# Kernel optimization log

Hardware: AMD Instinct MI355X
Metric: run time of the kernel (lower is better)

The kernel has to match this reference:

```python
import jax, jax.numpy as jnp
import numpy as np

OUT = 7               # adaptive max pool output size (7,7)
SPATIAL_SCALE = 1.0 / 16.0


def _adaptive_bins(offset, length, grid_len):
    """Boolean masks [OUT, grid_len] for AdaptiveMaxPool2d bin membership.

    Torch adaptive pooling: bin i covers [floor(i*L/OUT), ceil((i+1)*L/OUT)).
    offset/length are traced int32 scalars (ROI start and extent on the grid).
    """
    i = jnp.arange(OUT, dtype=jnp.int32)
    starts = offset + (i * length) // OUT                      # inclusive
    ends = offset + ((i + 1) * length + (OUT - 1)) // OUT      # exclusive (ceil)
    g = jnp.arange(grid_len, dtype=jnp.int32)
    return (g[None, :] >= starts[:, None]) & (g[None, :] < ends[:, None])


def _pool_one_roi(fmap, roi):
    """fmap: [C, H, W] float; roi: [4] int32 (x1, y1, x2, y2) in feature coords.

    Equivalent to features[:, :, y1:y2+1, x1:x2+1] followed by
    AdaptiveMaxPool2d((7,7)). Returns [C, OUT, OUT].
    """
    C, H, W = fmap.shape
    x1, y1, x2, y2 = roi[0], roi[1], roi[2], roi[3]
    h_len = y2 - y1 + 1   # torch slice y1:y2+1
    w_len = x2 - x1 + 1
    mask_h = _adaptive_bins(y1, h_len, H)   # [OUT, H]
    mask_w = _adaptive_bins(x1, w_len, W)   # [OUT, W]
    neg = jnp.finfo(fmap.dtype).min
    # reduce W first: [C, H, OUT]
    col = jnp.where(mask_w[None, None, :, :], fmap[:, :, None, :], neg).max(-1)
    # then reduce H: [C, OUT(h), OUT(w)]
    out = jnp.where(mask_h[None, :, :, None], col[:, None, :, :], neg).max(2)
    return out


def roi_pool(features, rois):
    # features: [1, C, H, W]; rois: [R, 4] int32 image-pixel (x1, y1, x2, y2)
    fmap = features[0]
    # rois.float().mul_(spatial_scale).long(): truncation == floor for coords >= 0
    rois_f = (rois.astype(features.dtype) * SPATIAL_SCALE).astype(jnp.int32)
    # sequential map over ROIs keeps the masked-max intermediate per-ROI sized
    return jax.lax.map(lambda r: _pool_one_roi(fmap, r), rois_f)  # [R, C, 7, 7]


def setup_inputs() -> dict:
    key = jax.random.key(0)
    k1, k2, k3, k4, k5 = jax.random.split(key, 5)
    C, H, W, R = 512, 64, 64, 1024
    features = jax.random.normal(k1, (1, C, H, W), dtype=jnp.float32)
    img = H * 16  # 1024 px image
    x1 = jax.random.randint(k2, (R,), 0, img - 128, dtype=jnp.int32)
    y1 = jax.random.randint(k3, (R,), 0, img - 128, dtype=jnp.int32)
    bw = jax.random.randint(k4, (R,), 16, 128, dtype=jnp.int32)
    bh = jax.random.randint(k5, (R,), 16, 128, dtype=jnp.int32)
    rois = jnp.stack([x1, y1, x1 + bw, y1 + bh], axis=1)  # [R, 4], in-bounds
    return {"features": features, "rois": rois}


def reference(features, rois):
    return roi_pool(features, rois)
```

## Files before the change

kernel.cpp:

```cpp
#include <hip/hip_runtime.h>
#include <float.h>

constexpr int CC = 512, HH = 64, WW = 64, HW = HH * WW;
#define NEG (-FLT_MAX)
typedef float f4 __attribute__((ext_vector_type(4)));

__global__ __launch_bounds__(256) void transpose_kernel(
    const float* __restrict__ f, float* __restrict__ ft)
{
    __shared__ float tile[64][65];
    int bc = blockIdx.x & 7;
    int bs = blockIdx.x >> 3;
    int tx = threadIdx.x & 63, ty0 = threadIdx.x >> 6;
#pragma unroll
    for (int k = 0; k < 16; ++k) {
        int c = k * 4 + ty0;
        tile[c][tx] = __builtin_nontemporal_load(
            &f[(size_t)(bc * 64 + c) * HW + bs * 64 + tx]);
    }
    __syncthreads();
#pragma unroll
    for (int k = 0; k < 16; ++k) {
        int s = k * 4 + ty0;
        ft[(size_t)(bs * 64 + s) * CC + bc * 64 + tx] = tile[tx][s];
    }
}

#define KMIN(j) ((2 * (j)) / 7)
#define KMAX(j) ((9 * ((j) + 1) + 6) / 7)

__global__ __launch_bounds__(256) void pool_kernel(
    const float* __restrict__ ft,
    const int4*  __restrict__ rois,
    float* __restrict__ out,
    int nblocks)
{
    __shared__ __align__(16) float lds[4][32 * 49];
    int wslot = threadIdx.x >> 6;
    int b = __builtin_amdgcn_readfirstlane(blockIdx.x);
    if (b >= nblocks) return;
    int lane = threadIdx.x & 63;

    int bc = b & 7;
    int g  = b >> 3;
    int r  = g * 4 + wslot;
    int c0 = bc << 6;

    int4 roi = rois[r];
    int x1 = roi.x >> 4, y1 = roi.y >> 4, x2 = roi.z >> 4, y2 = roi.w >> 4;
    int hl = y2 - y1 + 1, wl = x2 - x1 + 1;

    int hs[7], he[7], s_[7], e_[7];
#pragma unroll
    for (int i = 0; i < 7; ++i) {
        hs[i] = y1 + (i * hl) / 7;
        he[i] = y1 + ((i + 1) * hl + 6) / 7;
        s_[i] = (i * wl) / 7;
        e_[i] = ((i + 1) * wl + 6) / 7;
    }

    float acc[7][7];
#pragma unroll
    for (int i = 0; i < 7; ++i)
#pragma unroll
        for (int j = 0; j < 7; ++j) acc[i][j] = NEG;

    const float* fb = ft + c0 + lane;
    for (int h = y1; h <= y2; ++h) {
        const float* rowp = fb + (size_t)h * (WW * CC);
        float v[9];
#pragma unroll
        for (int k = 0; k < 9; ++k) {
            v[k] = NEG;
            if (k < wl)
                v[k] = rowp[(x1 + k) * CC];
        }
        float m[7];
#pragma unroll
        for (int j = 0; j < 7; ++j) {
            float a = NEG;
#pragma unroll
            for (int k = KMIN(j); k < KMAX(j); ++k) {
                bool p = (k >= s_[j]) && (k < e_[j]);
                a = fmaxf(a, p ? v[k] : NEG);
            }
            m[j] = a;
        }
#pragma unroll
        for (int i = 0; i < 7; ++i) {
            if (h >= hs[i] && h < he[i]) {
#pragma unroll
                for (int j = 0; j < 7; ++j)
                    acc[i][j] = fmaxf(acc[i][j], m[j]);
            }
        }
    }

    float* L  = lds[wslot];
    float* ob = out + ((size_t)r * CC + c0) * 49;
#pragma unroll
    for (int round = 0; round < 2; ++round) {
        if ((lane >> 5) == round) {
            float* p = L + (lane & 31) * 49;
#pragma unroll
            for (int i = 0; i < 7; ++i)
#pragma unroll
                for (int j = 0; j < 7; ++j) p[i * 7 + j] = acc[i][j];
        }
        asm volatile("s_waitcnt lgkmcnt(0)" ::: "memory");
        float* og = ob + round * 1568;
#pragma unroll
        for (int s = 0; s < 6; ++s) {
            int idx = s * 64 + lane;
            __builtin_nontemporal_store(*(const f4*)(L + idx * 4),
                                        (f4*)(og + idx * 4));
        }
        if (lane < 8) {
            int idx = 384 + lane;
            __builtin_nontemporal_store(*(const f4*)(L + idx * 4),
                                        (f4*)(og + idx * 4));
        }
        asm volatile("s_waitcnt lgkmcnt(0)" ::: "memory");
    }
}

__global__ __launch_bounds__(256) void roi_pool_direct(
    const float* __restrict__ features, const int4* __restrict__ rois,
    float* __restrict__ out, int ngroups)
{
    int wid = __builtin_amdgcn_readfirstlane(
        blockIdx.x * (blockDim.x >> 6) + (threadIdx.x >> 6));
    if (wid >= ngroups) return;
    int lane = threadIdx.x & 63;
    if (lane >= 49) return;
    int r = wid >> 4, c0 = (wid & 15) * 32;
    int4 roi = rois[r];
    int x1 = roi.x >> 4, y1 = roi.y >> 4, x2 = roi.z >> 4, y2 = roi.w >> 4;
    int h_len = y2 - y1 + 1, w_len = x2 - x1 + 1;
    int oh = lane / 7, ow = lane - oh * 7;
    int hs = y1 + (oh * h_len) / 7, he = y1 + ((oh + 1) * h_len + 6) / 7;
    int ws = x1 + (ow * w_len) / 7, we = x1 + ((ow + 1) * w_len + 6) / 7;
    int wlst = we - 1;
    int wa = ws, wb = min(ws + 1, wlst), wc = min(ws + 2, wlst);
    bool need1 = hs + 1 < he, need2 = hs + 2 < he;
    int o0 = (hs * WW + wa) * 4, o0b = (hs * WW + wb) * 4, o0c = (hs * WW + wc) * 4;
    const char* fb = (const char*)features + (size_t)c0 * (HW * 4);
    float* ob = out + ((size_t)r * CC + c0) * 49 + lane;
#pragma unroll 4
    for (int j = 0; j < 32; ++j) {
        float a = fmaxf(fmaxf(*(const float*)(fb + o0),
                              *(const float*)(fb + o0b)),
                        *(const float*)(fb + o0c));
        if (need1) {
            a = fmaxf(a, fmaxf(fmaxf(*(const float*)(fb + o0 + WW * 4),
                                     *(const float*)(fb + o0b + WW * 4)),
                               *(const float*)(fb + o0c + WW * 4)));
        }
        if (need2) {
            a = fmaxf(a, fmaxf(fmaxf(*(const float*)(fb + o0 + 2 * WW * 4),
                                     *(const float*)(fb + o0b + 2 * WW * 4)),
                               *(const float*)(fb + o0c + 2 * WW * 4)));
        }
        *ob = a;
        fb += HW * 4;
        ob += 49;
    }
}

extern "C" void kernel_launch(void* const* d_in, const int* in_sizes, int n_in,
                              void* d_out, int out_size, void* d_ws, size_t ws_size,
                              hipStream_t stream) {
    const float* features = (const float*)d_in[0];
    const int4*  rois     = (const int4*)d_in[1];
    float* out = (float*)d_out;
    int R = out_size / (CC * 49);

    if (ws_size >= (size_t)CC * HW * sizeof(float)) {
        float* ft = (float*)d_ws;
        transpose_kernel<<<512, 256, 0, stream>>>(features, ft);
        int nblocks = (R / 4) * 8;
        pool_kernel<<<nblocks, 256, 0, stream>>>(ft, rois, out, nblocks);
    } else {
        int ngroups = R * 16;
        roi_pool_direct<<<(ngroups + 3) / 4, 256, 0, stream>>>(features, rois, out, ngroups);
    }
}
```

Before: 33.80 us.

## Split pool wave over 32 channels and two row halves with shuffle merge

Each wave now handles 32 channels of one ROI instead of 64, and its two half-waves process alternating feature rows in parallel. The partial maxima are merged with a cross-half shuffle, and the output goes out in a single LDS staging round instead of two. This doubles the number of waves and roughly halves the serial row loop per wave, at the cost of a 49-element shuffle merge and half-wave (128-byte) loads per row. The block count is hardcoded to 4096, which matches only R=1024.

```diff
diff --git a/kernel.cpp b/kernel.cpp
--- a/kernel.cpp
+++ b/kernel.cpp
@@ -40,11 +40,15 @@
     int b = __builtin_amdgcn_readfirstlane(blockIdx.x);
     if (b >= nblocks) return;
     int lane = threadIdx.x & 63;
-
-    int bc = b & 7;
-    int g  = b >> 3;
-    int r  = g * 4 + wslot;
-    int c0 = bc << 6;
+    int ch   = lane & 31;
+    int half = lane >> 5;
+
+    int x = b & 7;
+    int g = b >> 3;
+    int u = g * 4 + wslot;
+    int r     = u >> 1;
+    int chunk = 2 * x + (u & 1);
+    int c0    = chunk << 5;
 
     int4 roi = rois[r];
     int x1 = roi.x >> 4, y1 = roi.y >> 4, x2 = roi.z >> 4, y2 = roi.w >> 4;
@@ -65,9 +69,14 @@
 #pragma unroll
         for (int j = 0; j < 7; ++j) acc[i][j] = NEG;
 
-    const float* fb = ft + c0 + lane;
-    for (int h = y1; h <= y2; ++h) {
-        const float* rowp = fb + (size_t)h * (WW * CC);
+    int loff_n = ch + half * (WW * CC);
+    int loff_l = (hl & 1) ? ch : loff_n;
+
+    int T = (hl + 1) >> 1;
+    for (int t = 0; t < T; ++t) {
+        int h0 = y1 + 2 * t;
+        const float* rowp = ft + c0 + (size_t)h0 * (WW * CC)
+                          + ((t == T - 1) ? loff_l : loff_n);
         float v[9];
 #pragma unroll
         for (int k = 0; k < 9; ++k) {
@@ -86,41 +95,48 @@
             }
             m[j] = a;
         }
+        int h = h0 + half;
 #pragma unroll
         for (int i = 0; i < 7; ++i) {
-            if (h >= hs[i] && h < he[i]) {
+            if (he[i] > h0 && hs[i] <= h0 + 1) {
+                bool in = (h >= hs[i]) && (h < he[i]);
 #pragma unroll
                 for (int j = 0; j < 7; ++j)
-                    acc[i][j] = fmaxf(acc[i][j], m[j]);
+                    acc[i][j] = fmaxf(acc[i][j], in ? m[j] : NEG);
             }
         }
     }
 
-    float* L  = lds[wslot];
-    float* ob = out + ((size_t)r * CC + c0) * 49;
-#pragma unroll
-    for (int round = 0; round < 2; ++round) {
-        if ((lane >> 5) == round) {
-            float* p = L + (lane & 31) * 49;
-#pragma unroll
-            for (int i = 0; i < 7; ++i)
-#pragma unroll
-                for (int j = 0; j < 7; ++j) p[i * 7 + j] = acc[i][j];
-        }
-        asm volatile("s_waitcnt lgkmcnt(0)" ::: "memory");
-        float* og = ob + round * 1568;
-#pragma unroll
-        for (int s = 0; s < 6; ++s) {
-            int idx = s * 64 + lane;
-            __builtin_nontemporal_store(*(const f4*)(L + idx * 4),
-                                        (f4*)(og + idx * 4));
-        }
-        if (lane < 8) {
-            int idx = 384 + lane;
-            __builtin_nontemporal_store(*(const f4*)(L + idx * 4),
-                                        (f4*)(og + idx * 4));
-        }
-        asm volatile("s_waitcnt lgkmcnt(0)" ::: "memory");
+#pragma unroll
+    for (int i = 0; i < 7; ++i)
+#pragma unroll
+        for (int j = 0; j < 7; ++j) {
+            float o = __shfl_xor(acc[i][j], 32, 64);
+            acc[i][j] = fmaxf(acc[i][j], o);
+        }
+
+    float* L = lds[wslot];
+#pragma unroll
+    for (int i = 0; i < 7; ++i) {
+        if ((i >= 4) == (half != 0)) {
+#pragma unroll
+            for (int j = 0; j < 7; ++j)
+                L[ch * 49 + i * 7 + j] = acc[i][j];
+        }
+    }
+    asm volatile("s_waitcnt lgkmcnt(0)" ::: "memory");
+
+    float* og = out + ((size_t)r * CC + c0) * 49;
+#pragma unroll
+    for (int s = 0; s < 6; ++s) {
+        int idx = s * 64 + lane;
+        __builtin_nontemporal_store(*(const f4*)(L + idx * 4),
+                                    (f4*)(og + idx * 4));
+    }
+    if (lane < 8) {
+        int idx = 384 + lane;
+        __builtin_nontemporal_store(*(const f4*)(L + idx * 4),
+                                    (f4*)(og + idx * 4));
     }
 }
 
@@ -178,7 +194,8 @@
     if (ws_size >= (size_t)CC * HW * sizeof(float)) {
         float* ft = (float*)d_ws;
         transpose_kernel<<<512, 256, 0, stream>>>(features, ft);
-        int nblocks = (R / 4) * 8;
+        int nblocks = (R * 16 / 2) / 4 * 2;
+        nblocks = 4096;
         pool_kernel<<<nblocks, 256, 0, stream>>>(ft, rois, out, nblocks);
     } else {
         int ngroups = R * 16;
```

After: 43.69 us. +29.2%, slower.
